# Kernel tuning notes

Measured on AMD Instinct MI355X. Metric: run time of the kernel, lower is better.

Reference implementation:

```python
import jax, jax.numpy as jnp
import numpy as np

N = 512      # n_res (act is a square pair representation [N, N, C])
C = 128      # act_dim / c_pair
I = 128      # num_intermediate_channel
EQUATION = 'ikc,jkc->ijc'  # 'outgoing' triangle multiplication
EPS = 1e-5

def _layernorm(x, g, b):
    mu = jnp.mean(x, axis=-1, keepdims=True)
    var = jnp.mean(jnp.square(x - mu), axis=-1, keepdims=True)
    return (x - mu) * jax.lax.rsqrt(var + EPS) * g + b

def setup_inputs() -> dict:
    key = jax.random.key(0)
    ks = jax.random.split(key, 12)
    s_c = 1.0 / np.sqrt(C)
    s_i = 1.0 / np.sqrt(I)
    return {
        'act': 0.1 * jax.random.normal(ks[0], (N, N, C), dtype=jnp.float32),
        'mask': (jax.random.uniform(ks[1], (N, N)) > 0.5).astype(jnp.float32),
        'ln_in_g': jnp.ones((C,), jnp.float32),
        'ln_in_b': jnp.zeros((C,), jnp.float32),
        'lp_w': s_c * jax.random.normal(ks[2], (C, I), jnp.float32),
        'lp_b': jnp.zeros((I,), jnp.float32),
        'rp_w': s_c * jax.random.normal(ks[3], (C, I), jnp.float32),
        'rp_b': jnp.zeros((I,), jnp.float32),
        'lg_w': s_c * jax.random.normal(ks[4], (C, I), jnp.float32),
        'lg_b': jnp.zeros((I,), jnp.float32),
        'rg_w': s_c * jax.random.normal(ks[5], (C, I), jnp.float32),
        'rg_b': jnp.zeros((I,), jnp.float32),
        'ln_c_g': jnp.ones((I,), jnp.float32),
        'ln_c_b': jnp.zeros((I,), jnp.float32),
        'out_w': s_i * jax.random.normal(ks[6], (I, C), jnp.float32),
        'out_b': jnp.zeros((C,), jnp.float32),
        'gate_w': s_c * jax.random.normal(ks[7], (C, C), jnp.float32),
        'gate_b': jnp.zeros((C,), jnp.float32),
    }

def reference(act, mask, ln_in_g, ln_in_b, lp_w, lp_b, rp_w, rp_b,
              lg_w, lg_b, rg_w, rg_b, ln_c_g, ln_c_b, out_w, out_b,
              gate_w, gate_b):
    m = mask[..., None]                                   # [N, N, 1]
    a = _layernorm(act, ln_in_g, ln_in_b)                 # input layernorm
    input_act = a
    # masked projections fused with sigmoid gates
    left = m * (a @ lp_w + lp_b) * jax.nn.sigmoid(a @ lg_w + lg_b)    # [N,N,I]
    right = m * (a @ rp_w + rp_b) * jax.nn.sigmoid(a @ rg_w + rg_b)   # [N,N,I]
    # triangle update: per-channel [N,N] x [N,N]^T matmul
    x = jnp.einsum(EQUATION, left, right)                 # [N,N,I]
    x = _layernorm(x, ln_c_g, ln_c_b)
    gate = jax.nn.sigmoid(input_act @ gate_w + gate_b)    # [N,N,C]
    return (x @ out_w + out_b) * gate
```

## Files before the change

### kernel.cpp

```cpp
#include <hip/hip_runtime.h>

#define NRES 512
#define N2   262144

typedef __attribute__((ext_vector_type(8))) short s16x8;
typedef __attribute__((ext_vector_type(4))) float f32x4;

__device__ __forceinline__ ushort f2bf(float x){
  union { float f; unsigned u; } v; v.f = x;
  unsigned r = (v.u + 0x7FFFu + ((v.u >> 16) & 1u)) >> 16;
  return (ushort)r;
}
__device__ __forceinline__ float bf2f(ushort h){
  union { unsigned u; float f; } v; v.u = ((unsigned)h) << 16; return v.f;
}
__device__ __forceinline__ unsigned pkbf(float lo, float hi){
  unsigned r;
  asm volatile("v_cvt_pk_bf16_f32 %0, %1, %2" : "=v"(r) : "v"(lo), "v"(hi));
  return r;
}
__device__ __forceinline__ float sigm(float x){ return 1.0f / (1.0f + __expf(-x)); }

__device__ __forceinline__ void gld_lds16(const void* g, void* lds){
  __builtin_amdgcn_global_load_lds((const __attribute__((address_space(1))) void*)g,
                                   (__attribute__((address_space(3))) void*)lds, 16, 0, 0);
}

#define VMCNT(n) asm volatile("s_waitcnt vmcnt(" #n ")" ::: "memory")

__global__ void k0_prep(const float* __restrict__ lp, const float* __restrict__ lg,
                        const float* __restrict__ rp, const float* __restrict__ rg,
                        const float* __restrict__ gw, const float* __restrict__ ow,
                        ushort* __restrict__ Wt)
{
  const float* srcs[6] = {lp, lg, rp, rg, gw, ow};
  const float* wsrc = srcs[blockIdx.x];
  ushort* dst = Wt + blockIdx.x * 16384;
  for (int f = threadIdx.x; f < 16384; f += blockDim.x){
    int n = f >> 7, k = f & 127;
    dst[f] = f2bf(wsrc[k * 128 + n]);
  }
}

__global__ __launch_bounds__(256) void k1a_ln(
    const float* __restrict__ act, const float* __restrict__ ln_g,
    const float* __restrict__ ln_b, ushort* __restrict__ a_ln)
{
  const int t = threadIdx.x;
  const int p0 = blockIdx.x * 128;
  const int g = t >> 5, j = t & 31;
  const float4 gv = *(const float4*)(ln_g + j * 4);
  const float4 bv = *(const float4*)(ln_b + j * 4);
  #pragma unroll
  for (int i = 0; i < 16; ++i){
    const int row = p0 + g + (i << 3);
    float4 v = *(const float4*)(act + (size_t)row * 128 + j * 4);
    float s = v.x + v.y + v.z + v.w;
    float q = v.x*v.x + v.y*v.y + v.z*v.z + v.w*v.w;
    #pragma unroll
    for (int m = 1; m < 32; m <<= 1){ s += __shfl_xor(s, m); q += __shfl_xor(q, m); }
    float mu = s * (1.0f / 128.0f);
    float rs = rsqrtf(q * (1.0f / 128.0f) - mu * mu + 1e-5f);
    uint2 o;
    o.x = pkbf((v.x - mu) * rs * gv.x + bv.x, (v.y - mu) * rs * gv.y + bv.y);
    o.y = pkbf((v.z - mu) * rs * gv.z + bv.z, (v.w - mu) * rs * gv.w + bv.w);
    *(uint2*)(a_ln + (size_t)row * 128 + j * 4) = o;
  }
}

__global__ __launch_bounds__(256) void k1b_proj(
    const ushort* __restrict__ a_ln, const float* __restrict__ mask,
    const float* __restrict__ lp_b, const float* __restrict__ lg_b,
    const float* __restrict__ rp_b, const float* __restrict__ rg_b,
    const float* __restrict__ gate_b, const ushort* __restrict__ Wt,
    ushort* __restrict__ leftg, ushort* __restrict__ rightg,
    ushort* __restrict__ gateg)
{
  __shared__ ushort Scr[4][16 * 72];
  const int t = threadIdx.x;
  const int p0 = blockIdx.x * 128;
  const int lane = t & 63, w = t >> 6;
  const int cl = lane & 15, h = lane >> 4;
  const float* Pb[3] = {lp_b, rp_b, gate_b};
  const float* Gb[2] = {lg_b, rg_b};
  ushort* dsts[3] = {leftg, rightg, gateg};
  ushort* scr = &Scr[w][0];
  const int rc = lane >> 2, rq = lane & 3;
  const f32x4 z = {0.f, 0.f, 0.f, 0.f};

  #pragma unroll
  for (int mh = 0; mh < 2; ++mh){
    s16x8 a[4][4];
    #pragma unroll
    for (int m = 0; m < 4; ++m)
      #pragma unroll
      for (int ks = 0; ks < 4; ++ks)
        a[m][ks] = *(const s16x8*)(a_ln + (size_t)(p0 + mh*64 + m*16 + cl) * 128
                                        + ks*32 + h*8);
    float mk[4][4];
    #pragma unroll
    for (int m = 0; m < 4; ++m)
      #pragma unroll
      for (int r = 0; r < 4; ++r)
        mk[m][r] = mask[p0 + mh*64 + m*16 + h*4 + r];

    for (int i = 0; i < 6; ++i){
      const int slab = w * 6 + i;
      const int out = slab >> 3;
      const int c0 = (slab & 7) << 4;
      const bool hasG = (out < 2);
      const ushort* WPp = Wt + (size_t)(out * 2) * 16384 + (size_t)(c0 + cl) * 128;
      s16x8 wfP[4], wfG[4];
      #pragma unroll
      for (int ks = 0; ks < 4; ++ks)
        wfP[ks] = *(const s16x8*)(WPp + ks*32 + h*8);
      if (hasG)
        #pragma unroll
        for (int ks = 0; ks < 4; ++ks)
          wfG[ks] = *(const s16x8*)(WPp + 16384 + ks*32 + h*8);
      const float pb = Pb[out][c0 + cl];
      const float gb = hasG ? Gb[out][c0 + cl] : 0.f;

      f32x4 accP[4], accG[4];
      #pragma unroll
      for (int m = 0; m < 4; ++m){ accP[m] = z; accG[m] = z; }
      #pragma unroll
      for (int ks = 0; ks < 4; ++ks)
        #pragma unroll
        for (int m = 0; m < 4; ++m)
          accP[m] = __builtin_amdgcn_mfma_f32_16x16x32_bf16(a[m][ks], wfP[ks], accP[m], 0, 0, 0);
      if (hasG){
        #pragma unroll
        for (int ks = 0; ks < 4; ++ks)
          #pragma unroll
          for (int m = 0; m < 4; ++m)
            accG[m] = __builtin_amdgcn_mfma_f32_16x16x32_bf16(a[m][ks], wfG[ks], accG[m], 0, 0, 0);
      }

      uint2 o[4];
      if (hasG){
        #pragma unroll
        for (int m = 0; m < 4; ++m){
          float x0 = mk[m][0] * (accP[m][0] + pb) * sigm(accG[m][0] + gb);
          float x1 = mk[m][1] * (accP[m][1] + pb) * sigm(accG[m][1] + gb);
          float x2 = mk[m][2] * (accP[m][2] + pb) * sigm(accG[m][2] + gb);
          float x3 = mk[m][3] * (accP[m][3] + pb) * sigm(accG[m][3] + gb);
          o[m].x = pkbf(x0, x1); o[m].y = pkbf(x2, x3);
        }
      } else {
        #pragma unroll
        for (int m = 0; m < 4; ++m){
          o[m].x = pkbf(sigm(accP[m][0] + pb), sigm(accP[m][1] + pb));
          o[m].y = pkbf(sigm(accP[m][2] + pb), sigm(accP[m][3] + pb));
        }
      }
      #pragma unroll
      for (int m = 0; m < 4; ++m)
        *(uint2*)&scr[cl * 72 + m * 16 + h * 4] = o[m];
      asm volatile("s_waitcnt lgkmcnt(0)" ::: "memory");
      ushort* dstg = dsts[out] + (size_t)c0 * N2 + p0 + mh * 64;
      s16x8 r0 = *(const s16x8*)&scr[rc * 72 + rq * 16];
      s16x8 r1 = *(const s16x8*)&scr[rc * 72 + rq * 16 + 8];
      *(s16x8*)(dstg + (size_t)rc * N2 + rq * 16)     = r0;
      *(s16x8*)(dstg + (size_t)rc * N2 + rq * 16 + 8) = r1;
    }
  }
}

__global__ __launch_bounds__(256) void k2_tri(const ushort* __restrict__ leftg,
                                              const ushort* __restrict__ rightg,
                                              ushort* __restrict__ X)
{
  __shared__ ushort Ab[3][128 * 32];
  __shared__ ushort Bb[3][128 * 32];
  const int t = threadIdx.x, lane = t & 63, w = t >> 6;
  const int b = blockIdx.x;
  const int c = b & 127, tile = b >> 7;
  const int tm = (tile >> 2) * 128, tn = (tile & 3) * 128;
  const char* Lc = (const char*)(leftg  + (size_t)c * N2);
  const char* Rc = (const char*)(rightg + (size_t)c * N2);
  ushort* Xc = X + (size_t)c * N2;
  const int wr = w >> 1, wc = w & 1, cl = lane & 15, h = lane >> 4;

  const int o0 = (w    ) * 1024 + lane * 16;
  const int o1 = (w + 4) * 1024 + lane * 16;
  const int row0 = o0 >> 6, row1 = o1 >> 6;
  const int sk0 = ((((o0 >> 4) & 3) ^ ((row0 >> 1) & 3)) << 4);
  const int sk1 = ((((o1 >> 4) & 3) ^ ((row1 >> 1) & 3)) << 4);

  f32x4 acc[4][4];
  const f32x4 z = {0.f, 0.f, 0.f, 0.f};
  #pragma unroll
  for (int m = 0; m < 4; ++m)
    #pragma unroll
    for (int n = 0; n < 4; ++n) acc[m][n] = z;

  auto stage = [&](int buf, int kt){
    gld_lds16(Lc + (size_t)(tm + row0) * 1024 + kt * 64 + sk0, (char*)&Ab[buf][0] + o0);
    gld_lds16(Lc + (size_t)(tm + row1) * 1024 + kt * 64 + sk1, (char*)&Ab[buf][0] + o1);
    gld_lds16(Rc + (size_t)(tn + row0) * 1024 + kt * 64 + sk0, (char*)&Bb[buf][0] + o0);
    gld_lds16(Rc + (size_t)(tn + row1) * 1024 + kt * 64 + sk1, (char*)&Bb[buf][0] + o1);
  };
  const int rsw = ((h ^ ((cl >> 1) & 3)) << 4);
  auto compute = [&](int buf){
    s16x8 a2[4], b2[4];
    #pragma unroll
    for (int m = 0; m < 4; ++m)
      a2[m] = *(const s16x8*)((const char*)&Ab[buf][0] + (wr*64 + m*16 + cl) * 64 + rsw);
    #pragma unroll
    for (int n = 0; n < 4; ++n)
      b2[n] = *(const s16x8*)((const char*)&Bb[buf][0] + (wc*64 + n*16 + cl) * 64 + rsw);
    #pragma unroll
    for (int m = 0; m < 4; ++m)
      #pragma unroll
      for (int n = 0; n < 4; ++n)
        acc[m][n] = __builtin_amdgcn_mfma_f32_16x16x32_bf16(a2[m], b2[n], acc[m][n], 0, 0, 0);
  };

  stage(0, 0);
  stage(1, 1);
  int cur = 0;
  for (int kt = 0; kt < 14; ++kt){
    VMCNT(4);
    __builtin_amdgcn_s_barrier();
    __builtin_amdgcn_sched_barrier(0);
    compute(cur);
    int nb = cur + 2; if (nb >= 3) nb -= 3;
    stage(nb, kt + 2);
    cur = (cur == 2) ? 0 : cur + 1;
  }
  VMCNT(4);
  __builtin_amdgcn_s_barrier();
  __builtin_amdgcn_sched_barrier(0);
  compute(cur);
  cur = (cur == 2) ? 0 : cur + 1;
  VMCNT(0);
  __builtin_amdgcn_s_barrier();
  __builtin_amdgcn_sched_barrier(0);
  compute(cur);

  #pragma unroll
  for (int m = 0; m < 4; ++m)
    #pragma unroll
    for (int n = 0; n < 4; ++n)
      #pragma unroll
      for (int r = 0; r < 4; ++r)
        Xc[(size_t)(tm + wr*64 + m*16 + h*4 + r) * NRES + tn + wc*64 + n*16 + cl] =
            f2bf(acc[m][n][r]);
}

__global__ __launch_bounds__(256) void k3_out(
    const ushort* __restrict__ X, const ushort* __restrict__ gateg,
    const ushort* __restrict__ Wt5,
    const float* __restrict__ ln_g, const float* __restrict__ ln_b,
    const float* __restrict__ ob, float* __restrict__ out)
{
  __shared__ ushort Alds[128 * 136];
  __shared__ ushort Wlds[128 * 136];
  __shared__ float part[8][2][128];
  __shared__ float stat[2][128];
  const int t = threadIdx.x;
  const int p0 = blockIdx.x * 128;
  const int g = t >> 5, j = t & 31;

  float4 xv[16];
  float s0 = 0, s1 = 0, s2 = 0, s3 = 0, q0 = 0, q1 = 0, q2 = 0, q3 = 0;
  #pragma unroll
  for (int i = 0; i < 16; ++i){
    const int cch = g + (i << 3);
    ushort4 u4 = *(const ushort4*)(X + (size_t)cch * N2 + p0 + j * 4);
    xv[i].x = bf2f(u4.x); xv[i].y = bf2f(u4.y);
    xv[i].z = bf2f(u4.z); xv[i].w = bf2f(u4.w);
    s0 += xv[i].x; q0 += xv[i].x * xv[i].x;
    s1 += xv[i].y; q1 += xv[i].y * xv[i].y;
    s2 += xv[i].z; q2 += xv[i].z * xv[i].z;
    s3 += xv[i].w; q3 += xv[i].w * xv[i].w;
  }
  part[g][0][j*4+0] = s0; part[g][0][j*4+1] = s1;
  part[g][0][j*4+2] = s2; part[g][0][j*4+3] = s3;
  part[g][1][j*4+0] = q0; part[g][1][j*4+1] = q1;
  part[g][1][j*4+2] = q2; part[g][1][j*4+3] = q3;
  __syncthreads();
  if (t < 128){
    float s = 0, q = 0;
    #pragma unroll
    for (int gg = 0; gg < 8; ++gg){ s += part[gg][0][t]; q += part[gg][1][t]; }
    float mu = s * (1.0f / 128.0f);
    float rs = rsqrtf(q * (1.0f / 128.0f) - mu * mu + 1e-5f);
    stat[0][t] = mu; stat[1][t] = rs;
  }
  __syncthreads();
  #pragma unroll
  for (int i = 0; i < 16; ++i){
    const int cch = g + (i << 3);
    const float gc = ln_g[cch], bc = ln_b[cch];
    const int p = j * 4;
    Alds[(p+0) * 136 + cch] = f2bf((xv[i].x - stat[0][p+0]) * stat[1][p+0] * gc + bc);
    Alds[(p+1) * 136 + cch] = f2bf((xv[i].y - stat[0][p+1]) * stat[1][p+1] * gc + bc);
    Alds[(p+2) * 136 + cch] = f2bf((xv[i].z - stat[0][p+2]) * stat[1][p+2] * gc + bc);
    Alds[(p+3) * 136 + cch] = f2bf((xv[i].w - stat[0][p+3]) * stat[1][p+3] * gc + bc);
  }
  #pragma unroll
  for (int u = 0; u < 8; ++u){
    int f = t + u * 256;
    int n = f >> 4, k8 = f & 15;
    *(s16x8*)&Wlds[n * 136 + k8 * 8] = *(const s16x8*)(Wt5 + f * 8);
  }
  __syncthreads();

  const int lane = t & 63, w = t >> 6;
  const int wr = w >> 1, wc = w & 1, cl = lane & 15, h = lane >> 4;
  f32x4 acc[4][4];
  const f32x4 z = {0.f, 0.f, 0.f, 0.f};
  #pragma unroll
  for (int m = 0; m < 4; ++m)
    #pragma unroll
    for (int n = 0; n < 4; ++n) acc[m][n] = z;
  #pragma unroll
  for (int ks = 0; ks < 4; ++ks){
    s16x8 a[4], bfr[4];
    #pragma unroll
    for (int m = 0; m < 4; ++m)
      a[m] = *(const s16x8*)&Alds[(wr*64 + m*16 + cl) * 136 + ks*32 + h*8];
    #pragma unroll
    for (int n = 0; n < 4; ++n)
      bfr[n] = *(const s16x8*)&Wlds[(wc*64 + n*16 + cl) * 136 + ks*32 + h*8];
    #pragma unroll
    for (int m = 0; m < 4; ++m)
      #pragma unroll
      for (int n = 0; n < 4; ++n)
        acc[m][n] = __builtin_amdgcn_mfma_f32_16x16x32_bf16(a[m], bfr[n], acc[m][n], 0, 0, 0);
  }

  float obv[4];
  #pragma unroll
  for (int n = 0; n < 4; ++n) obv[n] = ob[wc*64 + n*16 + cl];
  #pragma unroll
  for (int m = 0; m < 4; ++m)
    #pragma unroll
    for (int n = 0; n < 4; ++n){
      const int cc = wc*64 + n*16 + cl;
      ushort4 g4 = *(const ushort4*)(gateg + (size_t)cc * N2 + p0 + wr*64 + m*16 + h*4);
      const size_t pbase = p0 + wr*64 + m*16 + h*4;
      out[(pbase+0) * 128 + cc] = (acc[m][n][0] + obv[n]) * bf2f(g4.x);
      out[(pbase+1) * 128 + cc] = (acc[m][n][1] + obv[n]) * bf2f(g4.y);
      out[(pbase+2) * 128 + cc] = (acc[m][n][2] + obv[n]) * bf2f(g4.z);
      out[(pbase+3) * 128 + cc] = (acc[m][n][3] + obv[n]) * bf2f(g4.w);
    }
}

extern "C" void kernel_launch(void* const* d_in, const int* in_sizes, int n_in,
                              void* d_out, int out_size, void* d_ws, size_t ws_size,
                              hipStream_t stream)
{
  const float* act    = (const float*)d_in[0];
  const float* mask   = (const float*)d_in[1];
  const float* ln_in_g = (const float*)d_in[2];
  const float* ln_in_b = (const float*)d_in[3];
  const float* lp_w = (const float*)d_in[4];
  const float* lp_b = (const float*)d_in[5];
  const float* rp_w = (const float*)d_in[6];
  const float* rp_b = (const float*)d_in[7];
  const float* lg_w = (const float*)d_in[8];
  const float* lg_b = (const float*)d_in[9];
  const float* rg_w = (const float*)d_in[10];
  const float* rg_b = (const float*)d_in[11];
  const float* ln_c_g = (const float*)d_in[12];
  const float* ln_c_b = (const float*)d_in[13];
  const float* out_w  = (const float*)d_in[14];
  const float* out_b  = (const float*)d_in[15];
  const float* gate_w = (const float*)d_in[16];
  const float* gate_b = (const float*)d_in[17];
  float* outp = (float*)d_out;

  char* ws = (char*)d_ws;
  ushort* Wt     = (ushort*)(ws);
  ushort* a_ln   = (ushort*)(ws + 196608);
  ushort* leftg  = (ushort*)(ws + 196608 + 1ull * 67108864ull);
  ushort* rightg = (ushort*)(ws + 196608 + 2ull * 67108864ull);
  ushort* gateg  = (ushort*)(ws + 196608 + 3ull * 67108864ull);
  ushort* X      = (ushort*)(ws + 196608 + 4ull * 67108864ull);

  k0_prep<<<dim3(6), dim3(256), 0, stream>>>(lp_w, lg_w, rp_w, rg_w, gate_w, out_w, Wt);
  k1a_ln<<<dim3(2048), dim3(256), 0, stream>>>(act, ln_in_g, ln_in_b, a_ln);
  k1b_proj<<<dim3(2048), dim3(256), 0, stream>>>(a_ln, mask,
                                                 lp_b, lg_b, rp_b, rg_b, gate_b,
                                                 Wt, leftg, rightg, gateg);
  k2_tri<<<dim3(2048), dim3(256), 0, stream>>>(leftg, rightg, X);
  k3_out<<<dim3(2048), dim3(256), 0, stream>>>(X, gateg, Wt + 5 * 16384,
                                               ln_c_g, ln_c_b, out_b, outp);
}
```

Baseline: 539.3 us.

## Remap blocks across XCDs and stage tile stores and gate loads through LDS

Adds an XCD-aware block remapping so consecutive logical chunks land on the same XCD, aiming to improve L2 locality in all row-parallel kernels and the triangle matmul. In the triangle kernel, the output tile is written to LDS first and then stored with 16-byte row-contiguous writes instead of scattered 2-byte stores. In the output kernel, the gate tile is loaded coalesced into LDS before the epilogue rather than read with strided ushort4 loads. It also fully unrolls the projection slab loop. The cost is extra LDS traffic and barriers, plus higher register pressure from the unroll.

```diff
diff --git a/kernel.cpp b/kernel.cpp
--- a/kernel.cpp
+++ b/kernel.cpp
@@ -27,6 +27,10 @@
 }
 
 #define VMCNT(n) asm volatile("s_waitcnt vmcnt(" #n ")" ::: "memory")
+
+__device__ __forceinline__ int xcd_chunk(int bid){
+  return (bid & 7) * 256 + (bid >> 3);
+}
 
 __global__ void k0_prep(const float* __restrict__ lp, const float* __restrict__ lg,
                         const float* __restrict__ rp, const float* __restrict__ rg,
@@ -47,7 +51,7 @@
     const float* __restrict__ ln_b, ushort* __restrict__ a_ln)
 {
   const int t = threadIdx.x;
-  const int p0 = blockIdx.x * 128;
+  const int p0 = xcd_chunk(blockIdx.x) * 128;
   const int g = t >> 5, j = t & 31;
   const float4 gv = *(const float4*)(ln_g + j * 4);
   const float4 bv = *(const float4*)(ln_b + j * 4);
@@ -78,7 +82,7 @@
 {
   __shared__ ushort Scr[4][16 * 72];
   const int t = threadIdx.x;
-  const int p0 = blockIdx.x * 128;
+  const int p0 = xcd_chunk(blockIdx.x) * 128;
   const int lane = t & 63, w = t >> 6;
   const int cl = lane & 15, h = lane >> 4;
   const float* Pb[3] = {lp_b, rp_b, gate_b};
@@ -104,6 +108,7 @@
       for (int r = 0; r < 4; ++r)
         mk[m][r] = mask[p0 + mh*64 + m*16 + h*4 + r];
 
+    #pragma unroll
     for (int i = 0; i < 6; ++i){
       const int slab = w * 6 + i;
       const int out = slab >> 3;
@@ -171,11 +176,10 @@
                                               const ushort* __restrict__ rightg,
                                               ushort* __restrict__ X)
 {
-  __shared__ ushort Ab[3][128 * 32];
-  __shared__ ushort Bb[3][128 * 32];
+  __shared__ char smem[49152];
   const int t = threadIdx.x, lane = t & 63, w = t >> 6;
-  const int b = blockIdx.x;
-  const int c = b & 127, tile = b >> 7;
+  const int l = xcd_chunk(blockIdx.x);
+  const int c = l >> 4, tile = l & 15;
   const int tm = (tile >> 2) * 128, tn = (tile & 3) * 128;
   const char* Lc = (const char*)(leftg  + (size_t)c * N2);
   const char* Rc = (const char*)(rightg + (size_t)c * N2);
@@ -196,20 +200,24 @@
     for (int n = 0; n < 4; ++n) acc[m][n] = z;
 
   auto stage = [&](int buf, int kt){
-    gld_lds16(Lc + (size_t)(tm + row0) * 1024 + kt * 64 + sk0, (char*)&Ab[buf][0] + o0);
-    gld_lds16(Lc + (size_t)(tm + row1) * 1024 + kt * 64 + sk1, (char*)&Ab[buf][0] + o1);
-    gld_lds16(Rc + (size_t)(tn + row0) * 1024 + kt * 64 + sk0, (char*)&Bb[buf][0] + o0);
-    gld_lds16(Rc + (size_t)(tn + row1) * 1024 + kt * 64 + sk1, (char*)&Bb[buf][0] + o1);
+    char* Ab = smem + buf * 8192;
+    char* Bb = smem + 24576 + buf * 8192;
+    gld_lds16(Lc + (size_t)(tm + row0) * 1024 + kt * 64 + sk0, Ab + o0);
+    gld_lds16(Lc + (size_t)(tm + row1) * 1024 + kt * 64 + sk1, Ab + o1);
+    gld_lds16(Rc + (size_t)(tn + row0) * 1024 + kt * 64 + sk0, Bb + o0);
+    gld_lds16(Rc + (size_t)(tn + row1) * 1024 + kt * 64 + sk1, Bb + o1);
   };
   const int rsw = ((h ^ ((cl >> 1) & 3)) << 4);
   auto compute = [&](int buf){
+    const char* Ab = smem + buf * 8192;
+    const char* Bb = smem + 24576 + buf * 8192;
     s16x8 a2[4], b2[4];
     #pragma unroll
     for (int m = 0; m < 4; ++m)
-      a2[m] = *(const s16x8*)((const char*)&Ab[buf][0] + (wr*64 + m*16 + cl) * 64 + rsw);
+      a2[m] = *(const s16x8*)(Ab + (wr*64 + m*16 + cl) * 64 + rsw);
     #pragma unroll
     for (int n = 0; n < 4; ++n)
-      b2[n] = *(const s16x8*)((const char*)&Bb[buf][0] + (wc*64 + n*16 + cl) * 64 + rsw);
+      b2[n] = *(const s16x8*)(Bb + (wc*64 + n*16 + cl) * 64 + rsw);
     #pragma unroll
     for (int m = 0; m < 4; ++m)
       #pragma unroll
@@ -239,14 +247,23 @@
   __builtin_amdgcn_sched_barrier(0);
   compute(cur);
 
+  __syncthreads();
+  ushort* Xs = (ushort*)smem;
   #pragma unroll
   for (int m = 0; m < 4; ++m)
     #pragma unroll
     for (int n = 0; n < 4; ++n)
       #pragma unroll
       for (int r = 0; r < 4; ++r)
-        Xc[(size_t)(tm + wr*64 + m*16 + h*4 + r) * NRES + tn + wc*64 + n*16 + cl] =
-            f2bf(acc[m][n][r]);
+        Xs[(wr*64 + m*16 + h*4 + r) * 136 + wc*64 + n*16 + cl] = f2bf(acc[m][n][r]);
+  __syncthreads();
+  #pragma unroll
+  for (int v = 0; v < 8; ++v){
+    const int row = v * 16 + (t >> 4);
+    const int colb = (t & 15) * 8;
+    *(s16x8*)(Xc + (size_t)(tm + row) * NRES + tn + colb) =
+        *(const s16x8*)&Xs[row * 136 + colb];
+  }
 }
 
 __global__ __launch_bounds__(256) void k3_out(
@@ -260,7 +277,7 @@
   __shared__ float part[8][2][128];
   __shared__ float stat[2][128];
   const int t = threadIdx.x;
-  const int p0 = blockIdx.x * 128;
+  const int p0 = xcd_chunk(blockIdx.x) * 128;
   const int g = t >> 5, j = t & 31;
 
   float4 xv[16];
@@ -332,6 +349,21 @@
         acc[m][n] = __builtin_amdgcn_mfma_f32_16x16x32_bf16(a[m], bfr[n], acc[m][n], 0, 0, 0);
   }
 
+  __syncthreads();
+  {
+    const int cch = t & 127, prt = t >> 7;
+    const ushort* gp = gateg + (size_t)cch * N2 + p0 + prt * 64;
+    #pragma unroll
+    for (int u = 0; u < 8; ++u){
+      union { s16x8 v; ushort e[8]; } gv;
+      gv.v = *(const s16x8*)(gp + u * 8);
+      #pragma unroll
+      for (int e8 = 0; e8 < 8; ++e8)
+        Alds[(prt*64 + u*8 + e8) * 136 + cch] = gv.e[e8];
+    }
+  }
+  __syncthreads();
+
   float obv[4];
   #pragma unroll
   for (int n = 0; n < 4; ++n) obv[n] = ob[wc*64 + n*16 + cl];
@@ -340,12 +372,13 @@
     #pragma unroll
     for (int n = 0; n < 4; ++n){
       const int cc = wc*64 + n*16 + cl;
-      ushort4 g4 = *(const ushort4*)(gateg + (size_t)cc * N2 + p0 + wr*64 + m*16 + h*4);
-      const size_t pbase = p0 + wr*64 + m*16 + h*4;
-      out[(pbase+0) * 128 + cc] = (acc[m][n][0] + obv[n]) * bf2f(g4.x);
-      out[(pbase+1) * 128 + cc] = (acc[m][n][1] + obv[n]) * bf2f(g4.y);
-      out[(pbase+2) * 128 + cc] = (acc[m][n][2] + obv[n]) * bf2f(g4.z);
-      out[(pbase+3) * 128 + cc] = (acc[m][n][3] + obv[n]) * bf2f(g4.w);
+      const int rl = wr*64 + m*16 + h*4;
+      const size_t pbase = p0 + rl;
+      #pragma unroll
+      for (int r = 0; r < 4; ++r){
+        float gf = bf2f(Alds[(rl + r) * 136 + cc]);
+        out[(pbase + r) * 128 + cc] = (acc[m][n][r] + obv[n]) * gf;
+      }
     }
 }
 
```

After: 580.9 us. 1.08x slower.
